# Kernel tuning notes

Hardware: AMD Instinct MI355X
Metric: run time of the kernel (lower is better)

## Reference

```python
import jax, jax.numpy as jnp
import numpy as np
from itertools import combinations

B, NC, ORDER, H1, H2, CLS = 2048, 32, 2, 64, 32, 10
M = 496  # C(32,2)
EPS = 1e-5


def setup_inputs() -> dict:
    key = jax.random.key(0)
    ks = jax.random.split(key, 20)
    pair_idx = jnp.asarray(np.array(list(combinations(range(NC), ORDER)), dtype=np.int64))  # [M,2]
    bnd1 = 1.0 / np.sqrt(ORDER)
    bnd2 = 1.0 / np.sqrt(H1)
    bnd3 = 1.0 / np.sqrt(H2)
    bndo = 1.0 / np.sqrt(M)
    u = lambda k, shp, b: jax.random.uniform(k, shp, jnp.float32, -b, b)
    return {
        "x": jax.random.normal(ks[0], (B, NC), jnp.float32),
        "pair_idx": pair_idx,
        "W1": u(ks[1], (M, H1, ORDER), bnd1), "b1": u(ks[2], (M, H1), bnd1),
        "g1": 1.0 + 0.1 * jax.random.normal(ks[3], (M, H1), jnp.float32),
        "be1": 0.1 * jax.random.normal(ks[4], (M, H1), jnp.float32),
        "m1": 0.1 * jax.random.normal(ks[5], (M, H1), jnp.float32),
        "v1": 0.5 + jax.random.uniform(ks[6], (M, H1), jnp.float32),
        "W2": u(ks[7], (M, H2, H1), bnd2), "b2": u(ks[8], (M, H2), bnd2),
        "g2": 1.0 + 0.1 * jax.random.normal(ks[9], (M, H2), jnp.float32),
        "be2": 0.1 * jax.random.normal(ks[10], (M, H2), jnp.float32),
        "m2": 0.1 * jax.random.normal(ks[11], (M, H2), jnp.float32),
        "v2": 0.5 + jax.random.uniform(ks[12], (M, H2), jnp.float32),
        "W3": u(ks[13], (M, 1, H2), bnd3), "b3": u(ks[14], (M, 1), bnd3),
        "Wout": u(ks[15], (CLS, M), bndo), "bout": u(ks[16], (CLS,), bndo),
    }


def reference(x, pair_idx, W1, b1, g1, be1, m1, v1, W2, b2, g2, be2, m2, v2, W3, b3, Wout, bout):
    # gather pairs: [B, M, order]  (== input[:, nary_indices])
    h = x[:, pair_idx]
    # grouped 1x1 conv == per-group matmul; BN in eval mode with running stats
    h = jnp.einsum('bmi,moi->bmo', h, W1) + b1
    h = jax.nn.relu(g1 * (h - m1) * jax.lax.rsqrt(v1 + EPS) + be1)
    h = jnp.einsum('bmi,moi->bmo', h, W2) + b2
    h = jax.nn.relu(g2 * (h - m2) * jax.lax.rsqrt(v2 + EPS) + be2)
    o = (jnp.einsum('bmi,moi->bmo', h, W3) + b3)[..., 0]  # [B, M]
    return o @ Wout.T + bout  # [B, CLS]
```

## Files before the change

kernel.cpp:

```cpp
#include <hip/hip_runtime.h>
#include <hip/hip_bf16.h>

#define B_    2048
#define NC_   32
#define H1_   64
#define H2_   32
#define CLS_  10
#define M_    496
#define EPS_  1e-5f

typedef __attribute__((ext_vector_type(8))) short bf16x8;
typedef __attribute__((ext_vector_type(4))) float f32x4;

union F8 { int4 i; bf16x8 h; };

__device__ __forceinline__ short f2bf(float f) {
    unsigned u = __float_as_uint(f);
    u = (u + 0x7FFFu + ((u >> 16) & 1u)) >> 16;
    return (short)u;
}

__device__ __forceinline__ unsigned pack_bf2(float e, float o) {
    unsigned ue = __float_as_uint(e) + 0x8000u;
    unsigned uo = __float_as_uint(o) + 0x8000u;
    return __builtin_amdgcn_perm(uo, ue, 0x07060302u);
}

__device__ __forceinline__ void pair_of_m(int m, int& i0, int& i1) {
    int a = 0, rem = m;
    while (rem >= (NC_ - 1 - a)) { rem -= (NC_ - 1 - a); ++a; }
    i0 = a; i1 = a + 1 + rem;
}

#define OBUF_BYTES  ((size_t)M_ * B_ * 4)
#define W2A_BYTES   ((size_t)M_ * 2 * 2 * 64 * 16)

__global__ __launch_bounds__(256) void k_prep(
    const float* __restrict__ W2, int4* __restrict__ W2a)
{
    int t = blockIdx.x * 256 + threadIdx.x;
    int lane = t & 63, s = (t >> 6) & 1, u = (t >> 7) & 1, m = t >> 8;
    int q = lane >> 4, ln = lane & 15;
    const float* p = W2 + m * (H2_ * H1_) + (u * 16 + ln) * H1_ + s * 32 + q * 8;
    float4 f0 = *(const float4*)p;
    float4 f1 = *(const float4*)(p + 4);
    int4 d;
    d.x = ((unsigned)(unsigned short)f2bf(f0.x)) | ((unsigned)(unsigned short)f2bf(f0.y) << 16);
    d.y = ((unsigned)(unsigned short)f2bf(f0.z)) | ((unsigned)(unsigned short)f2bf(f0.w) << 16);
    d.z = ((unsigned)(unsigned short)f2bf(f1.x)) | ((unsigned)(unsigned short)f2bf(f1.y) << 16);
    d.w = ((unsigned)(unsigned short)f2bf(f1.z)) | ((unsigned)(unsigned short)f2bf(f1.w) << 16);
    W2a[t] = d;
}

template <bool PREP>
__global__ __launch_bounds__(256) void k_main2(
    const float* __restrict__ x,
    const float* __restrict__ W1, const float* __restrict__ b1,
    const float* __restrict__ g1, const float* __restrict__ be1,
    const float* __restrict__ m1, const float* __restrict__ v1,
    const float* __restrict__ W2, const int4* __restrict__ W2a,
    const float* __restrict__ b2p,
    const float* __restrict__ g2, const float* __restrict__ be2,
    const float* __restrict__ m2, const float* __restrict__ v2,
    const float* __restrict__ W3, const float* __restrict__ b3,
    float* __restrict__ obuf)
{
    __shared__ float w1aS[H1_], w1bS[H1_], c1S[H1_];
    __shared__ float s2S[H2_], c2S[H2_], w3S[H2_];
    __shared__ float xs0[256], xs1[256];

    const int m   = blockIdx.x;
    const int tid = threadIdx.x;

    int i0, i1;
    pair_of_m(m, i0, i1);

    if (tid < H1_) {
        int j = m * H1_ + tid;
        float s = g1[j] * rsqrtf(v1[j] + EPS_);
        w1aS[tid] = s * W1[2 * j];
        w1bS[tid] = s * W1[2 * j + 1];
        c1S[tid]  = fmaf(s, b1[j] - m1[j], be1[j]);
    } else if (tid < H1_ + H2_) {
        int o = tid - H1_;
        int j = m * H2_ + o;
        float s = g2[j] * rsqrtf(v2[j] + EPS_);
        s2S[o] = s;
        c2S[o] = fmaf(s, b2p[j] - m2[j], be2[j]);
        w3S[o] = W3[j];
    }
    {
        int b = blockIdx.y * 256 + tid;
        xs0[tid] = x[b * NC_ + i0];
        xs1[tid] = x[b * NC_ + i1];
    }
    __syncthreads();

    const int lane = tid & 63;
    const int w    = tid >> 6;
    const int q    = lane >> 4;
    const int ln   = lane & 15;
    const int wbase = w * 64;
    const float b3m = b3[m];

    F8 wfr[2][2];
    if (PREP) {
        const int4* p = W2a + (m * 4) * 64 + lane;
#pragma unroll
        for (int u = 0; u < 2; ++u)
#pragma unroll
            for (int s = 0; s < 2; ++s)
                wfr[u][s].i = p[(u * 2 + s) * 64];
    } else {
        const float* W2m = W2 + m * (H2_ * H1_);
#pragma unroll
        for (int u = 0; u < 2; ++u)
#pragma unroll
            for (int s = 0; s < 2; ++s) {
                const float* p = W2m + (u * 16 + ln) * H1_ + s * 32 + q * 8;
                float4 f0 = *(const float4*)p;
                float4 f1 = *(const float4*)(p + 4);
                int4 d;
                d.x = ((unsigned)(unsigned short)f2bf(f0.x)) | ((unsigned)(unsigned short)f2bf(f0.y) << 16);
                d.y = ((unsigned)(unsigned short)f2bf(f0.z)) | ((unsigned)(unsigned short)f2bf(f0.w) << 16);
                d.z = ((unsigned)(unsigned short)f2bf(f1.x)) | ((unsigned)(unsigned short)f2bf(f1.y) << 16);
                d.w = ((unsigned)(unsigned short)f2bf(f1.z)) | ((unsigned)(unsigned short)f2bf(f1.w) << 16);
                wfr[u][s].i = d;
            }
    }

    float x0v[4], x1v[4];
#pragma unroll
    for (int t = 0; t < 4; ++t) {
        x0v[t] = xs0[wbase + t * 16 + ln];
        x1v[t] = xs1[wbase + t * 16 + ln];
    }

    float s2a0[4], c2a0[4], w3a0[4], s2a1[4], c2a1[4], w3a1[4];
#pragma unroll
    for (int r = 0; r < 4; ++r) {
        int n0 = q * 4 + r, n1 = 16 + n0;
        s2a0[r] = s2S[n0]; c2a0[r] = c2S[n0]; w3a0[r] = w3S[n0];
        s2a1[r] = s2S[n1]; c2a1[r] = c2S[n1]; w3a1[r] = w3S[n1];
    }

    F8 hfr[4][2];
#pragma unroll
    for (int s = 0; s < 2; ++s)
#pragma unroll
        for (int jp = 0; jp < 4; ++jp) {
            int ke = s * 32 + q * 8 + 2 * jp;
            float wae = w1aS[ke],     wbe = w1bS[ke],     ce = c1S[ke];
            float wao = w1aS[ke + 1], wbo = w1bS[ke + 1], co = c1S[ke + 1];
            unsigned dw[4];
#pragma unroll
            for (int t = 0; t < 4; ++t) {
                float he = fmaxf(fmaf(x0v[t], wae, fmaf(x1v[t], wbe, ce)), 0.f);
                float ho = fmaxf(fmaf(x0v[t], wao, fmaf(x1v[t], wbo, co)), 0.f);
                dw[t] = pack_bf2(he, ho);
            }
            hfr[0][s].i[jp] = dw[0];  hfr[1][s].i[jp] = dw[1];
            hfr[2][s].i[jp] = dw[2];  hfr[3][s].i[jp] = dw[3];
        }

    float ot[4];
#pragma unroll
    for (int t = 0; t < 4; ++t) {
        f32x4 acc0 = {0.f, 0.f, 0.f, 0.f};
        f32x4 acc1 = {0.f, 0.f, 0.f, 0.f};
        acc0 = __builtin_amdgcn_mfma_f32_16x16x32_bf16(wfr[0][0].h, hfr[t][0].h, acc0, 0, 0, 0);
        acc0 = __builtin_amdgcn_mfma_f32_16x16x32_bf16(wfr[0][1].h, hfr[t][1].h, acc0, 0, 0, 0);
        acc1 = __builtin_amdgcn_mfma_f32_16x16x32_bf16(wfr[1][0].h, hfr[t][0].h, acc1, 0, 0, 0);
        acc1 = __builtin_amdgcn_mfma_f32_16x16x32_bf16(wfr[1][1].h, hfr[t][1].h, acc1, 0, 0, 0);

        float part = 0.f;
#pragma unroll
        for (int r = 0; r < 4; ++r) {
            float h20 = fmaxf(fmaf(s2a0[r], acc0[r], c2a0[r]), 0.f);
            float h21 = fmaxf(fmaf(s2a1[r], acc1[r], c2a1[r]), 0.f);
            part = fmaf(h20, w3a0[r], fmaf(h21, w3a1[r], part));
        }
        part += __shfl_xor(part, 16, 64);
        part += __shfl_xor(part, 32, 64);
        ot[t] = part;
    }

    float o = (q == 0) ? ot[0] : (q == 1) ? ot[1] : (q == 2) ? ot[2] : ot[3];
    obuf[m * B_ + blockIdx.y * 256 + wbase + lane] = o + b3m;
}

__global__ __launch_bounds__(256) void k_out(
    const float* __restrict__ obuf, const float* __restrict__ Wout,
    const float* __restrict__ bout, float* __restrict__ out)
{
    __shared__ float red[256 * CLS_];
    const int tid = threadIdx.x;
    const int bl  = tid & 31;
    const int mg  = tid >> 5;
    const int b   = blockIdx.x * 32 + bl;

    float acc[CLS_];
#pragma unroll
    for (int c = 0; c < CLS_; ++c) acc[c] = 0.f;

#pragma unroll 4
    for (int m = mg; m < M_; m += 8) {
        float o = obuf[m * B_ + b];
#pragma unroll
        for (int c = 0; c < CLS_; ++c)
            acc[c] = fmaf(o, Wout[c * M_ + m], acc[c]);
    }
#pragma unroll
    for (int c = 0; c < CLS_; ++c) red[tid * CLS_ + c] = acc[c];
    __syncthreads();

    if (mg == 0) {
#pragma unroll
        for (int c = 0; c < CLS_; ++c) {
            float s = bout[c];
#pragma unroll
            for (int g = 0; g < 8; ++g)
                s += red[(g * 32 + bl) * CLS_ + c];
            out[b * CLS_ + c] = s;
        }
    }
}

__global__ __launch_bounds__(256) void k_fused(
    const float* __restrict__ x,
    const float* __restrict__ W1, const float* __restrict__ b1,
    const float* __restrict__ g1, const float* __restrict__ be1,
    const float* __restrict__ m1, const float* __restrict__ v1,
    const float* __restrict__ W2, const float* __restrict__ b2p,
    const float* __restrict__ g2, const float* __restrict__ be2,
    const float* __restrict__ m2, const float* __restrict__ v2,
    const float* __restrict__ W3, const float* __restrict__ b3,
    const float* __restrict__ Wout, const float* __restrict__ bout,
    float* __restrict__ out)
{
    __shared__ float red[256 * CLS_];
    const int tid = threadIdx.x;
    const int bl  = tid & 7;
    const int mg  = tid >> 3;
    const int b   = blockIdx.x * 8 + bl;

    float acc[CLS_];
#pragma unroll
    for (int c = 0; c < CLS_; ++c) acc[c] = 0.f;

    for (int m = mg; m < M_; m += 32) {
        int i0, i1;
        pair_of_m(m, i0, i1);
        const float x0 = x[b * NC_ + i0];
        const float x1 = x[b * NC_ + i1];

        float h1[H1_];
#pragma unroll
        for (int o = 0; o < H1_; ++o) {
            int j = m * H1_ + o;
            float s = g1[j] * rsqrtf(v1[j] + EPS_);
            float pre = fmaf(x0, s * W1[2 * j],
                        fmaf(x1, s * W1[2 * j + 1],
                             fmaf(s, b1[j] - m1[j], be1[j])));
            h1[o] = fmaxf(pre, 0.f);
        }
        float acc3 = b3[m];
#pragma unroll 2
        for (int o = 0; o < H2_; ++o) {
            int j = m * H2_ + o;
            const float* __restrict__ r = W2 + j * H1_;
            float d = 0.f;
#pragma unroll
            for (int i = 0; i < H1_; ++i) d = fmaf(h1[i], r[i], d);
            float s = g2[j] * rsqrtf(v2[j] + EPS_);
            float h2 = fmaxf(fmaf(s, d + b2p[j] - m2[j], be2[j]), 0.f);
            acc3 = fmaf(h2, W3[j], acc3);
        }
#pragma unroll
        for (int c = 0; c < CLS_; ++c)
            acc[c] = fmaf(acc3, Wout[c * M_ + m], acc[c]);
    }

#pragma unroll
    for (int c = 0; c < CLS_; ++c) red[tid * CLS_ + c] = acc[c];
    __syncthreads();

    if (mg == 0) {
#pragma unroll
        for (int c = 0; c < CLS_; ++c) {
            float s = bout[c];
            for (int g = 0; g < 32; ++g)
                s += red[(g * 8 + bl) * CLS_ + c];
            out[b * CLS_ + c] = s;
        }
    }
}

extern "C" void kernel_launch(void* const* d_in, const int* in_sizes, int n_in,
                              void* d_out, int out_size, void* d_ws, size_t ws_size,
                              hipStream_t stream)
{
    const float* x    = (const float*)d_in[0];
    const float* W1   = (const float*)d_in[2];
    const float* b1   = (const float*)d_in[3];
    const float* g1   = (const float*)d_in[4];
    const float* be1  = (const float*)d_in[5];
    const float* m1   = (const float*)d_in[6];
    const float* v1   = (const float*)d_in[7];
    const float* W2   = (const float*)d_in[8];
    const float* b2p  = (const float*)d_in[9];
    const float* g2   = (const float*)d_in[10];
    const float* be2  = (const float*)d_in[11];
    const float* m2   = (const float*)d_in[12];
    const float* v2   = (const float*)d_in[13];
    const float* W3   = (const float*)d_in[14];
    const float* b3   = (const float*)d_in[15];
    const float* Wout = (const float*)d_in[16];
    const float* bout = (const float*)d_in[17];
    float* out  = (float*)d_out;
    float* obuf = (float*)d_ws;
    int4*  W2a  = (int4*)((char*)d_ws + OBUF_BYTES);

    if (ws_size >= OBUF_BYTES + W2A_BYTES) {
        k_prep<<<M_, 256, 0, stream>>>(W2, W2a);
        k_main2<true><<<dim3(M_, B_ / 256), 256, 0, stream>>>(
            x, W1, b1, g1, be1, m1, v1, W2, W2a,
            b2p, g2, be2, m2, v2, W3, b3, obuf);
        k_out<<<B_ / 32, 256, 0, stream>>>(obuf, Wout, bout, out);
    } else if (ws_size >= OBUF_BYTES) {
        k_main2<false><<<dim3(M_, B_ / 256), 256, 0, stream>>>(
            x, W1, b1, g1, be1, m1, v1, W2, (const int4*)nullptr,
            b2p, g2, be2, m2, v2, W3, b3, obuf);
        k_out<<<B_ / 32, 256, 0, stream>>>(obuf, Wout, bout, out);
    } else {
        k_fused<<<B_ / 8, 256, 0, stream>>>(
            x, W1, b1, g1, be1, m1, v1,
            W2, b2p, g2, be2, m2, v2, W3, b3, Wout, bout, out);
    }
}
```

Baseline: 121.6 us.

## Double batch per main block and split output GEMV into chunked partials

The main kernel now handles 512 batch rows per block in two halves. This halves the grid and amortizes the per-pair parameter setup and W2 fragment loads over twice the work. The output projection is split across 16 chunks of pairs into a partial buffer, followed by a small final reduction kernel that adds the bias. The aim is more parallelism in the output stage than the old 64-block kernel gave. The cost is an extra launch and more workspace, and the default path only runs if the workspace is large enough.

Result: faster. 116.5 us, median of 2 (-4.2%).

```diff
diff --git a/kernel.cpp b/kernel.cpp
--- a/kernel.cpp
+++ b/kernel.cpp
@@ -34,6 +34,8 @@
 
 #define OBUF_BYTES  ((size_t)M_ * B_ * 4)
 #define W2A_BYTES   ((size_t)M_ * 2 * 2 * 64 * 16)
+#define NCHUNK 16
+#define PBUF_BYTES  ((size_t)NCHUNK * B_ * CLS_ * 4)
 
 __global__ __launch_bounds__(256) void k_prep(
     const float* __restrict__ W2, int4* __restrict__ W2a)
@@ -53,7 +55,7 @@
 }
 
 template <bool PREP>
-__global__ __launch_bounds__(256) void k_main2(
+__global__ __launch_bounds__(256) void k_main3(
     const float* __restrict__ x,
     const float* __restrict__ W1, const float* __restrict__ b1,
     const float* __restrict__ g1, const float* __restrict__ be1,
@@ -67,7 +69,7 @@
 {
     __shared__ float w1aS[H1_], w1bS[H1_], c1S[H1_];
     __shared__ float s2S[H2_], c2S[H2_], w3S[H2_];
-    __shared__ float xs0[256], xs1[256];
+    __shared__ float xs0[512], xs1[512];
 
     const int m   = blockIdx.x;
     const int tid = threadIdx.x;
@@ -90,9 +92,11 @@
         w3S[o] = W3[j];
     }
     {
-        int b = blockIdx.y * 256 + tid;
-        xs0[tid] = x[b * NC_ + i0];
-        xs1[tid] = x[b * NC_ + i1];
+        int bb = blockIdx.y * 512;
+        xs0[tid]       = x[(bb + tid) * NC_ + i0];
+        xs1[tid]       = x[(bb + tid) * NC_ + i1];
+        xs0[256 + tid] = x[(bb + 256 + tid) * NC_ + i0];
+        xs1[256 + tid] = x[(bb + 256 + tid) * NC_ + i1];
     }
     __syncthreads();
 
@@ -100,7 +104,7 @@
     const int w    = tid >> 6;
     const int q    = lane >> 4;
     const int ln   = lane & 15;
-    const int wbase = w * 64;
+    const int wbase = w * 128;
     const float b3m = b3[m];
 
     F8 wfr[2][2];
@@ -129,13 +133,6 @@
             }
     }
 
-    float x0v[4], x1v[4];
-#pragma unroll
-    for (int t = 0; t < 4; ++t) {
-        x0v[t] = xs0[wbase + t * 16 + ln];
-        x1v[t] = xs1[wbase + t * 16 + ln];
-    }
-
     float s2a0[4], c2a0[4], w3a0[4], s2a1[4], c2a1[4], w3a1[4];
 #pragma unroll
     for (int r = 0; r < 4; ++r) {
@@ -144,52 +141,113 @@
         s2a1[r] = s2S[n1]; c2a1[r] = c2S[n1]; w3a1[r] = w3S[n1];
     }
 
-    F8 hfr[4][2];
-#pragma unroll
-    for (int s = 0; s < 2; ++s)
-#pragma unroll
-        for (int jp = 0; jp < 4; ++jp) {
-            int ke = s * 32 + q * 8 + 2 * jp;
-            float wae = w1aS[ke],     wbe = w1bS[ke],     ce = c1S[ke];
-            float wao = w1aS[ke + 1], wbo = w1bS[ke + 1], co = c1S[ke + 1];
-            unsigned dw[4];
-#pragma unroll
-            for (int t = 0; t < 4; ++t) {
-                float he = fmaxf(fmaf(x0v[t], wae, fmaf(x1v[t], wbe, ce)), 0.f);
-                float ho = fmaxf(fmaf(x0v[t], wao, fmaf(x1v[t], wbo, co)), 0.f);
-                dw[t] = pack_bf2(he, ho);
+#pragma unroll
+    for (int h = 0; h < 2; ++h) {
+        const int hbase = wbase + h * 64;
+
+        float x0v[4], x1v[4];
+#pragma unroll
+        for (int t = 0; t < 4; ++t) {
+            x0v[t] = xs0[hbase + t * 16 + ln];
+            x1v[t] = xs1[hbase + t * 16 + ln];
+        }
+
+        F8 hfr[4][2];
+#pragma unroll
+        for (int s = 0; s < 2; ++s)
+#pragma unroll
+            for (int jp = 0; jp < 4; ++jp) {
+                int ke = s * 32 + q * 8 + 2 * jp;
+                float wae = w1aS[ke],     wbe = w1bS[ke],     ce = c1S[ke];
+                float wao = w1aS[ke + 1], wbo = w1bS[ke + 1], co = c1S[ke + 1];
+                unsigned dw[4];
+#pragma unroll
+                for (int t = 0; t < 4; ++t) {
+                    float he = fmaxf(fmaf(x0v[t], wae, fmaf(x1v[t], wbe, ce)), 0.f);
+                    float ho = fmaxf(fmaf(x0v[t], wao, fmaf(x1v[t], wbo, co)), 0.f);
+                    dw[t] = pack_bf2(he, ho);
+                }
+                hfr[0][s].i[jp] = dw[0];  hfr[1][s].i[jp] = dw[1];
+                hfr[2][s].i[jp] = dw[2];  hfr[3][s].i[jp] = dw[3];
             }
-            hfr[0][s].i[jp] = dw[0];  hfr[1][s].i[jp] = dw[1];
-            hfr[2][s].i[jp] = dw[2];  hfr[3][s].i[jp] = dw[3];
-        }
-
-    float ot[4];
-#pragma unroll
-    for (int t = 0; t < 4; ++t) {
-        f32x4 acc0 = {0.f, 0.f, 0.f, 0.f};
-        f32x4 acc1 = {0.f, 0.f, 0.f, 0.f};
-        acc0 = __builtin_amdgcn_mfma_f32_16x16x32_bf16(wfr[0][0].h, hfr[t][0].h, acc0, 0, 0, 0);
-        acc0 = __builtin_amdgcn_mfma_f32_16x16x32_bf16(wfr[0][1].h, hfr[t][1].h, acc0, 0, 0, 0);
-        acc1 = __builtin_amdgcn_mfma_f32_16x16x32_bf16(wfr[1][0].h, hfr[t][0].h, acc1, 0, 0, 0);
-        acc1 = __builtin_amdgcn_mfma_f32_16x16x32_bf16(wfr[1][1].h, hfr[t][1].h, acc1, 0, 0, 0);
-
-        float part = 0.f;
-#pragma unroll
-        for (int r = 0; r < 4; ++r) {
-            float h20 = fmaxf(fmaf(s2a0[r], acc0[r], c2a0[r]), 0.f);
-            float h21 = fmaxf(fmaf(s2a1[r], acc1[r], c2a1[r]), 0.f);
-            part = fmaf(h20, w3a0[r], fmaf(h21, w3a1[r], part));
-        }
-        part += __shfl_xor(part, 16, 64);
-        part += __shfl_xor(part, 32, 64);
-        ot[t] = part;
-    }
-
-    float o = (q == 0) ? ot[0] : (q == 1) ? ot[1] : (q == 2) ? ot[2] : ot[3];
-    obuf[m * B_ + blockIdx.y * 256 + wbase + lane] = o + b3m;
-}
-
-__global__ __launch_bounds__(256) void k_out(
+
+        float ot[4];
+#pragma unroll
+        for (int t = 0; t < 4; ++t) {
+            f32x4 acc0 = {0.f, 0.f, 0.f, 0.f};
+            f32x4 acc1 = {0.f, 0.f, 0.f, 0.f};
+            acc0 = __builtin_amdgcn_mfma_f32_16x16x32_bf16(wfr[0][0].h, hfr[t][0].h, acc0, 0, 0, 0);
+            acc0 = __builtin_amdgcn_mfma_f32_16x16x32_bf16(wfr[0][1].h, hfr[t][1].h, acc0, 0, 0, 0);
+            acc1 = __builtin_amdgcn_mfma_f32_16x16x32_bf16(wfr[1][0].h, hfr[t][0].h, acc1, 0, 0, 0);
+            acc1 = __builtin_amdgcn_mfma_f32_16x16x32_bf16(wfr[1][1].h, hfr[t][1].h, acc1, 0, 0, 0);
+
+            float part = 0.f;
+#pragma unroll
+            for (int r = 0; r < 4; ++r) {
+                float h20 = fmaxf(fmaf(s2a0[r], acc0[r], c2a0[r]), 0.f);
+                float h21 = fmaxf(fmaf(s2a1[r], acc1[r], c2a1[r]), 0.f);
+                part = fmaf(h20, w3a0[r], fmaf(h21, w3a1[r], part));
+            }
+            part += __shfl_xor(part, 16, 64);
+            part += __shfl_xor(part, 32, 64);
+            ot[t] = part;
+        }
+
+        float o = (q == 0) ? ot[0] : (q == 1) ? ot[1] : (q == 2) ? ot[2] : ot[3];
+        obuf[m * B_ + blockIdx.y * 512 + hbase + lane] = o + b3m;
+    }
+}
+
+__global__ __launch_bounds__(256) void k_outp(
+    const float* __restrict__ obuf, const float* __restrict__ Wout,
+    float* __restrict__ pbuf)
+{
+    __shared__ float red[256 * CLS_];
+    const int tid = threadIdx.x;
+    const int bl  = tid & 63;
+    const int mg  = tid >> 6;
+    const int b   = blockIdx.x * 64 + bl;
+    const int mb  = blockIdx.y * 31;
+
+    float acc[CLS_];
+#pragma unroll
+    for (int c = 0; c < CLS_; ++c) acc[c] = 0.f;
+
+    for (int i = mg; i < 31; i += 4) {
+        int m = mb + i;
+        float o = obuf[m * B_ + b];
+#pragma unroll
+        for (int c = 0; c < CLS_; ++c)
+            acc[c] = fmaf(o, Wout[c * M_ + m], acc[c]);
+    }
+#pragma unroll
+    for (int c = 0; c < CLS_; ++c) red[tid * CLS_ + c] = acc[c];
+    __syncthreads();
+
+    if (mg == 0) {
+#pragma unroll
+        for (int c = 0; c < CLS_; ++c) {
+            float s = red[(0 * 64 + bl) * CLS_ + c] + red[(1 * 64 + bl) * CLS_ + c]
+                    + red[(2 * 64 + bl) * CLS_ + c] + red[(3 * 64 + bl) * CLS_ + c];
+            pbuf[(blockIdx.y * B_ + b) * CLS_ + c] = s;
+        }
+    }
+}
+
+__global__ __launch_bounds__(256) void k_fin(
+    const float* __restrict__ pbuf, const float* __restrict__ bout,
+    float* __restrict__ out)
+{
+    int t = blockIdx.x * 256 + threadIdx.x;
+    int c = t % CLS_;
+    float s = bout[c];
+#pragma unroll
+    for (int ch = 0; ch < NCHUNK; ++ch)
+        s += pbuf[ch * (B_ * CLS_) + t];
+    out[t] = s;
+}
+
+__global__ __launch_bounds__(256) void k_out1(
     const float* __restrict__ obuf, const float* __restrict__ Wout,
     const float* __restrict__ bout, float* __restrict__ out)
 {
@@ -202,7 +260,6 @@
     float acc[CLS_];
 #pragma unroll
     for (int c = 0; c < CLS_; ++c) acc[c] = 0.f;
-
 #pragma unroll 4
     for (int m = mg; m < M_; m += 8) {
         float o = obuf[m * B_ + b];
@@ -213,7 +270,6 @@
 #pragma unroll
     for (int c = 0; c < CLS_; ++c) red[tid * CLS_ + c] = acc[c];
     __syncthreads();
-
     if (mg == 0) {
 #pragma unroll
         for (int c = 0; c < CLS_; ++c) {
@@ -253,7 +309,6 @@
         pair_of_m(m, i0, i1);
         const float x0 = x[b * NC_ + i0];
         const float x1 = x[b * NC_ + i1];
-
         float h1[H1_];
 #pragma unroll
         for (int o = 0; o < H1_; ++o) {
@@ -284,7 +339,6 @@
 #pragma unroll
     for (int c = 0; c < CLS_; ++c) red[tid * CLS_ + c] = acc[c];
     __syncthreads();
-
     if (mg == 0) {
 #pragma unroll
         for (int c = 0; c < CLS_; ++c) {
@@ -320,18 +374,20 @@
     float* out  = (float*)d_out;
     float* obuf = (float*)d_ws;
     int4*  W2a  = (int4*)((char*)d_ws + OBUF_BYTES);
-
-    if (ws_size >= OBUF_BYTES + W2A_BYTES) {
+    float* pbuf = (float*)((char*)d_ws + OBUF_BYTES + W2A_BYTES);
+
+    if (ws_size >= OBUF_BYTES + W2A_BYTES + PBUF_BYTES) {
         k_prep<<<M_, 256, 0, stream>>>(W2, W2a);
-        k_main2<true><<<dim3(M_, B_ / 256), 256, 0, stream>>>(
+        k_main3<true><<<dim3(M_, B_ / 512), 256, 0, stream>>>(
             x, W1, b1, g1, be1, m1, v1, W2, W2a,
             b2p, g2, be2, m2, v2, W3, b3, obuf);
-        k_out<<<B_ / 32, 256, 0, stream>>>(obuf, Wout, bout, out);
+        k_outp<<<dim3(B_ / 64, NCHUNK), 256, 0, stream>>>(obuf, Wout, pbuf);
+        k_fin<<<(B_ * CLS_) / 256, 256, 0, stream>>>(pbuf, bout, out);
     } else if (ws_size >= OBUF_BYTES) {
-        k_main2<false><<<dim3(M_, B_ / 256), 256, 0, stream>>>(
+        k_main3<false><<<dim3(M_, B_ / 512), 256, 0, stream>>>(
             x, W1, b1, g1, be1, m1, v1, W2, (const int4*)nullptr,
             b2p, g2, be2, m2, v2, W3, b3, obuf);
-        k_out<<<B_ / 32, 256, 0, stream>>>(obuf, Wout, bout, out);
+        k_out1<<<B_ / 32, 256, 0, stream>>>(obuf, Wout, bout, out);
     } else {
         k_fused<<<B_ / 8, 256, 0, stream>>>(
             x, W1, b1, g1, be1, m1, v1,
```

## Drop W2 prep kernel, double batch per block, split output GEMV over M with atomics

Applied to the files above, without the earlier changes.

Removes the separate W2 bf16 prep kernel and converts W2 inline in the main kernel. Each block now handles 512 batch rows, so the per-m weight conversion and BN folding are amortized over twice the work. Blocks with m==0 initialize the output with the bias. The final Wout projection is split across 16 M-chunks of 31 with atomicAdd accumulation, giving more parallelism. This risks atomic contention and relies on the main kernel's bias write finishing before the projection kernel runs, which stream ordering provides.

Measured after the change: 128.8 us. 5.9% more time.

```diff
diff --git a/kernel.cpp b/kernel.cpp
--- a/kernel.cpp
+++ b/kernel.cpp
@@ -33,44 +33,34 @@
 }
 
 #define OBUF_BYTES  ((size_t)M_ * B_ * 4)
-#define W2A_BYTES   ((size_t)M_ * 2 * 2 * 64 * 16)
-
-__global__ __launch_bounds__(256) void k_prep(
-    const float* __restrict__ W2, int4* __restrict__ W2a)
-{
-    int t = blockIdx.x * 256 + threadIdx.x;
-    int lane = t & 63, s = (t >> 6) & 1, u = (t >> 7) & 1, m = t >> 8;
-    int q = lane >> 4, ln = lane & 15;
-    const float* p = W2 + m * (H2_ * H1_) + (u * 16 + ln) * H1_ + s * 32 + q * 8;
-    float4 f0 = *(const float4*)p;
-    float4 f1 = *(const float4*)(p + 4);
-    int4 d;
-    d.x = ((unsigned)(unsigned short)f2bf(f0.x)) | ((unsigned)(unsigned short)f2bf(f0.y) << 16);
-    d.y = ((unsigned)(unsigned short)f2bf(f0.z)) | ((unsigned)(unsigned short)f2bf(f0.w) << 16);
-    d.z = ((unsigned)(unsigned short)f2bf(f1.x)) | ((unsigned)(unsigned short)f2bf(f1.y) << 16);
-    d.w = ((unsigned)(unsigned short)f2bf(f1.z)) | ((unsigned)(unsigned short)f2bf(f1.w) << 16);
-    W2a[t] = d;
-}
-
-template <bool PREP>
-__global__ __launch_bounds__(256) void k_main2(
+
+__global__ __launch_bounds__(256) void k_main3(
     const float* __restrict__ x,
     const float* __restrict__ W1, const float* __restrict__ b1,
     const float* __restrict__ g1, const float* __restrict__ be1,
     const float* __restrict__ m1, const float* __restrict__ v1,
-    const float* __restrict__ W2, const int4* __restrict__ W2a,
-    const float* __restrict__ b2p,
+    const float* __restrict__ W2, const float* __restrict__ b2p,
     const float* __restrict__ g2, const float* __restrict__ be2,
     const float* __restrict__ m2, const float* __restrict__ v2,
     const float* __restrict__ W3, const float* __restrict__ b3,
-    float* __restrict__ obuf)
+    const float* __restrict__ bout,
+    float* __restrict__ obuf, float* __restrict__ out)
 {
     __shared__ float w1aS[H1_], w1bS[H1_], c1S[H1_];
     __shared__ float s2S[H2_], c2S[H2_], w3S[H2_];
-    __shared__ float xs0[256], xs1[256];
+    __shared__ float xs0[512], xs1[512];
 
     const int m   = blockIdx.x;
     const int tid = threadIdx.x;
+
+    if (m == 0) {
+        const int base = blockIdx.y * (B_ / 4) * CLS_;
+#pragma unroll
+        for (int k = 0; k < (B_ / 4) * CLS_ / 256; ++k) {
+            int idx = tid + k * 256;
+            out[base + idx] = bout[idx % CLS_];
+        }
+    }
 
     int i0, i1;
     pair_of_m(m, i0, i1);
@@ -90,9 +80,11 @@
         w3S[o] = W3[j];
     }
     {
-        int b = blockIdx.y * 256 + tid;
-        xs0[tid] = x[b * NC_ + i0];
-        xs1[tid] = x[b * NC_ + i1];
+        int bb = blockIdx.y * 512;
+        xs0[tid]       = x[(bb + tid) * NC_ + i0];
+        xs1[tid]       = x[(bb + tid) * NC_ + i1];
+        xs0[256 + tid] = x[(bb + 256 + tid) * NC_ + i0];
+        xs1[256 + tid] = x[(bb + 256 + tid) * NC_ + i1];
     }
     __syncthreads();
 
@@ -100,18 +92,11 @@
     const int w    = tid >> 6;
     const int q    = lane >> 4;
     const int ln   = lane & 15;
-    const int wbase = w * 64;
+    const int wbase = w * 128;
     const float b3m = b3[m];
 
     F8 wfr[2][2];
-    if (PREP) {
-        const int4* p = W2a + (m * 4) * 64 + lane;
-#pragma unroll
-        for (int u = 0; u < 2; ++u)
-#pragma unroll
-            for (int s = 0; s < 2; ++s)
-                wfr[u][s].i = p[(u * 2 + s) * 64];
-    } else {
+    {
         const float* W2m = W2 + m * (H2_ * H1_);
 #pragma unroll
         for (int u = 0; u < 2; ++u)
@@ -121,19 +106,12 @@
                 float4 f0 = *(const float4*)p;
                 float4 f1 = *(const float4*)(p + 4);
                 int4 d;
-                d.x = ((unsigned)(unsigned short)f2bf(f0.x)) | ((unsigned)(unsigned short)f2bf(f0.y) << 16);
-                d.y = ((unsigned)(unsigned short)f2bf(f0.z)) | ((unsigned)(unsigned short)f2bf(f0.w) << 16);
-                d.z = ((unsigned)(unsigned short)f2bf(f1.x)) | ((unsigned)(unsigned short)f2bf(f1.y) << 16);
-                d.w = ((unsigned)(unsigned short)f2bf(f1.z)) | ((unsigned)(unsigned short)f2bf(f1.w) << 16);
+                d.x = (unsigned)(unsigned short)f2bf(f0.x) | ((unsigned)(unsigned short)f2bf(f0.y) << 16);
+                d.y = (unsigned)(unsigned short)f2bf(f0.z) | ((unsigned)(unsigned short)f2bf(f0.w) << 16);
+                d.z = (unsigned)(unsigned short)f2bf(f1.x) | ((unsigned)(unsigned short)f2bf(f1.y) << 16);
+                d.w = (unsigned)(unsigned short)f2bf(f1.z) | ((unsigned)(unsigned short)f2bf(f1.w) << 16);
                 wfr[u][s].i = d;
             }
-    }
-
-    float x0v[4], x1v[4];
-#pragma unroll
-    for (int t = 0; t < 4; ++t) {
-        x0v[t] = xs0[wbase + t * 16 + ln];
-        x1v[t] = xs1[wbase + t * 16 + ln];
     }
 
     float s2a0[4], c2a0[4], w3a0[4], s2a1[4], c2a1[4], w3a1[4];
@@ -144,67 +122,80 @@
         s2a1[r] = s2S[n1]; c2a1[r] = c2S[n1]; w3a1[r] = w3S[n1];
     }
 
-    F8 hfr[4][2];
-#pragma unroll
-    for (int s = 0; s < 2; ++s)
-#pragma unroll
-        for (int jp = 0; jp < 4; ++jp) {
-            int ke = s * 32 + q * 8 + 2 * jp;
-            float wae = w1aS[ke],     wbe = w1bS[ke],     ce = c1S[ke];
-            float wao = w1aS[ke + 1], wbo = w1bS[ke + 1], co = c1S[ke + 1];
-            unsigned dw[4];
-#pragma unroll
-            for (int t = 0; t < 4; ++t) {
-                float he = fmaxf(fmaf(x0v[t], wae, fmaf(x1v[t], wbe, ce)), 0.f);
-                float ho = fmaxf(fmaf(x0v[t], wao, fmaf(x1v[t], wbo, co)), 0.f);
-                dw[t] = pack_bf2(he, ho);
+#pragma unroll
+    for (int h = 0; h < 2; ++h) {
+        const int hbase = wbase + h * 64;
+
+        float x0v[4], x1v[4];
+#pragma unroll
+        for (int t = 0; t < 4; ++t) {
+            x0v[t] = xs0[hbase + t * 16 + ln];
+            x1v[t] = xs1[hbase + t * 16 + ln];
+        }
+
+        F8 hfr[4][2];
+#pragma unroll
+        for (int s = 0; s < 2; ++s)
+#pragma unroll
+            for (int jp = 0; jp < 4; ++jp) {
+                int ke = s * 32 + q * 8 + 2 * jp;
+                float wae = w1aS[ke],     wbe = w1bS[ke],     ce = c1S[ke];
+                float wao = w1aS[ke + 1], wbo = w1bS[ke + 1], co = c1S[ke + 1];
+                unsigned dw[4];
+#pragma unroll
+                for (int t = 0; t < 4; ++t) {
+                    float he = fmaxf(fmaf(x0v[t], wae, fmaf(x1v[t], wbe, ce)), 0.f);
+                    float ho = fmaxf(fmaf(x0v[t], wao, fmaf(x1v[t], wbo, co)), 0.f);
+                    dw[t] = pack_bf2(he, ho);
+                }
+                hfr[0][s].i[jp] = dw[0];  hfr[1][s].i[jp] = dw[1];
+                hfr[2][s].i[jp] = dw[2];  hfr[3][s].i[jp] = dw[3];
             }
-            hfr[0][s].i[jp] = dw[0];  hfr[1][s].i[jp] = dw[1];
-            hfr[2][s].i[jp] = dw[2];  hfr[3][s].i[jp] = dw[3];
-        }
-
-    float ot[4];
-#pragma unroll
-    for (int t = 0; t < 4; ++t) {
-        f32x4 acc0 = {0.f, 0.f, 0.f, 0.f};
-        f32x4 acc1 = {0.f, 0.f, 0.f, 0.f};
-        acc0 = __builtin_amdgcn_mfma_f32_16x16x32_bf16(wfr[0][0].h, hfr[t][0].h, acc0, 0, 0, 0);
-        acc0 = __builtin_amdgcn_mfma_f32_16x16x32_bf16(wfr[0][1].h, hfr[t][1].h, acc0, 0, 0, 0);
-        acc1 = __builtin_amdgcn_mfma_f32_16x16x32_bf16(wfr[1][0].h, hfr[t][0].h, acc1, 0, 0, 0);
-        acc1 = __builtin_amdgcn_mfma_f32_16x16x32_bf16(wfr[1][1].h, hfr[t][1].h, acc1, 0, 0, 0);
-
-        float part = 0.f;
-#pragma unroll
-        for (int r = 0; r < 4; ++r) {
-            float h20 = fmaxf(fmaf(s2a0[r], acc0[r], c2a0[r]), 0.f);
-            float h21 = fmaxf(fmaf(s2a1[r], acc1[r], c2a1[r]), 0.f);
-            part = fmaf(h20, w3a0[r], fmaf(h21, w3a1[r], part));
-        }
-        part += __shfl_xor(part, 16, 64);
-        part += __shfl_xor(part, 32, 64);
-        ot[t] = part;
-    }
-
-    float o = (q == 0) ? ot[0] : (q == 1) ? ot[1] : (q == 2) ? ot[2] : ot[3];
-    obuf[m * B_ + blockIdx.y * 256 + wbase + lane] = o + b3m;
-}
-
-__global__ __launch_bounds__(256) void k_out(
+
+        float ot[4];
+#pragma unroll
+        for (int t = 0; t < 4; ++t) {
+            f32x4 acc0 = {0.f, 0.f, 0.f, 0.f};
+            f32x4 acc1 = {0.f, 0.f, 0.f, 0.f};
+            acc0 = __builtin_amdgcn_mfma_f32_16x16x32_bf16(wfr[0][0].h, hfr[t][0].h, acc0, 0, 0, 0);
+            acc0 = __builtin_amdgcn_mfma_f32_16x16x32_bf16(wfr[0][1].h, hfr[t][1].h, acc0, 0, 0, 0);
+            acc1 = __builtin_amdgcn_mfma_f32_16x16x32_bf16(wfr[1][0].h, hfr[t][0].h, acc1, 0, 0, 0);
+            acc1 = __builtin_amdgcn_mfma_f32_16x16x32_bf16(wfr[1][1].h, hfr[t][1].h, acc1, 0, 0, 0);
+
+            float part = 0.f;
+#pragma unroll
+            for (int r = 0; r < 4; ++r) {
+                float h20 = fmaxf(fmaf(s2a0[r], acc0[r], c2a0[r]), 0.f);
+                float h21 = fmaxf(fmaf(s2a1[r], acc1[r], c2a1[r]), 0.f);
+                part = fmaf(h20, w3a0[r], fmaf(h21, w3a1[r], part));
+            }
+            part += __shfl_xor(part, 16, 64);
+            part += __shfl_xor(part, 32, 64);
+            ot[t] = part;
+        }
+
+        float o = (q == 0) ? ot[0] : (q == 1) ? ot[1] : (q == 2) ? ot[2] : ot[3];
+        obuf[m * B_ + blockIdx.y * 512 + hbase + lane] = o + b3m;
+    }
+}
+
+__global__ __launch_bounds__(256) void k_outa(
     const float* __restrict__ obuf, const float* __restrict__ Wout,
-    const float* __restrict__ bout, float* __restrict__ out)
+    float* __restrict__ out)
 {
     __shared__ float red[256 * CLS_];
     const int tid = threadIdx.x;
-    const int bl  = tid & 31;
-    const int mg  = tid >> 5;
-    const int b   = blockIdx.x * 32 + bl;
+    const int bl  = tid & 63;
+    const int mg  = tid >> 6;
+    const int b   = blockIdx.x * 64 + bl;
+    const int mb  = blockIdx.y * 31;
 
     float acc[CLS_];
 #pragma unroll
     for (int c = 0; c < CLS_; ++c) acc[c] = 0.f;
 
-#pragma unroll 4
-    for (int m = mg; m < M_; m += 8) {
+    for (int i = mg; i < 31; i += 4) {
+        int m = mb + i;
         float o = obuf[m * B_ + b];
 #pragma unroll
         for (int c = 0; c < CLS_; ++c)
@@ -217,11 +208,9 @@
     if (mg == 0) {
 #pragma unroll
         for (int c = 0; c < CLS_; ++c) {
-            float s = bout[c];
-#pragma unroll
-            for (int g = 0; g < 8; ++g)
-                s += red[(g * 32 + bl) * CLS_ + c];
-            out[b * CLS_ + c] = s;
+            float s = red[(0 * 64 + bl) * CLS_ + c] + red[(1 * 64 + bl) * CLS_ + c]
+                    + red[(2 * 64 + bl) * CLS_ + c] + red[(3 * 64 + bl) * CLS_ + c];
+            atomicAdd(out + b * CLS_ + c, s);
         }
     }
 }
@@ -253,7 +242,6 @@
         pair_of_m(m, i0, i1);
         const float x0 = x[b * NC_ + i0];
         const float x1 = x[b * NC_ + i1];
-
         float h1[H1_];
 #pragma unroll
         for (int o = 0; o < H1_; ++o) {
@@ -284,7 +272,6 @@
 #pragma unroll
     for (int c = 0; c < CLS_; ++c) red[tid * CLS_ + c] = acc[c];
     __syncthreads();
-
     if (mg == 0) {
 #pragma unroll
         for (int c = 0; c < CLS_; ++c) {
@@ -319,19 +306,12 @@
     const float* bout = (const float*)d_in[17];
     float* out  = (float*)d_out;
     float* obuf = (float*)d_ws;
-    int4*  W2a  = (int4*)((char*)d_ws + OBUF_BYTES);
-
-    if (ws_size >= OBUF_BYTES + W2A_BYTES) {
-        k_prep<<<M_, 256, 0, stream>>>(W2, W2a);
-        k_main2<true><<<dim3(M_, B_ / 256), 256, 0, stream>>>(
-            x, W1, b1, g1, be1, m1, v1, W2, W2a,
-            b2p, g2, be2, m2, v2, W3, b3, obuf);
-        k_out<<<B_ / 32, 256, 0, stream>>>(obuf, Wout, bout, out);
-    } else if (ws_size >= OBUF_BYTES) {
-        k_main2<false><<<dim3(M_, B_ / 256), 256, 0, stream>>>(
-            x, W1, b1, g1, be1, m1, v1, W2, (const int4*)nullptr,
-            b2p, g2, be2, m2, v2, W3, b3, obuf);
-        k_out<<<B_ / 32, 256, 0, stream>>>(obuf, Wout, bout, out);
+
+    if (ws_size >= OBUF_BYTES) {
+        k_main3<<<dim3(M_, B_ / 512), 256, 0, stream>>>(
+            x, W1, b1, g1, be1, m1, v1, W2, b2p, g2, be2, m2, v2,
+            W3, b3, bout, obuf, out);
+        k_outa<<<dim3(B_ / 64, 16), 256, 0, stream>>>(obuf, Wout, out);
     } else {
         k_fused<<<B_ / 8, 256, 0, stream>>>(
             x, W1, b1, g1, be1, m1, v1,
```
